# Kernel optimization log

Measured on AMD Instinct MI355X. Metric: run time of the kernel, lower is better.

Reference implementation:

```python
import jax, jax.numpy as jnp
import numpy as np

IN_CHANNELS = 192
KERNEL_SIZE = 3
GROUPS = 1
N_ITER = 3  # power_it_niter


def _gram_conv(K):
    """Gram step of the conv operator: G[a, b] = sum_o corr(K[o, a], K[o, b]).

    K: (co, ci, k, k) -> (ci, ci, 2k-1, 2k-1). This is the kernel of M^T M
    where M is the (zero-padded) conv operator with kernel K.
    """
    k = K.shape[-1]
    lhs = jnp.transpose(K, (1, 0, 2, 3))  # batch = a-index, channels = o
    rhs = jnp.transpose(K, (1, 0, 2, 3))  # out-chan = b-index, in-chan = o
    return jax.lax.conv_general_dilated(
        lhs, rhs, window_strides=(1, 1),
        padding=[(k - 1, k - 1), (k - 1, k - 1)],
        dimension_numbers=("NCHW", "OIHW", "NCHW"))


def _sigma_one_group(K, n_iter):
    """Gram-iteration spectral-norm estimate (Delattre et al. 2024).

    sigma(K_0) ~= prod_t f_t^(1/2^t) * ||K_T||_F^(1/2^T), f_t = Frobenius norm
    before each Gram squaring (normalization keeps values in fp range).
    """
    log_sigma = jnp.asarray(0.0, K.dtype)
    for t in range(n_iter):  # static unroll: kernel spatial size grows k -> 2k-1
        f = jnp.sqrt(jnp.sum(K * K))
        K = K / f
        log_sigma = log_sigma + jnp.log(f) / (2.0 ** t)
        K = _gram_conv(K)
    f_final = jnp.sqrt(jnp.sum(K * K))
    log_sigma = log_sigma + jnp.log(f_final) / (2.0 ** n_iter)
    return jnp.exp(log_sigma)


def compute_delattre2024(K, n_iter):
    # K: (groups, c, c, k, k) -> (groups,) per-group spectral norm estimates
    return jax.vmap(lambda g: _sigma_one_group(g, n_iter))(K)


def setup_inputs() -> dict:
    key = jax.random.key(0)
    kernel = jax.random.normal(
        key, (IN_CHANNELS * GROUPS, IN_CHANNELS, KERNEL_SIZE, KERNEL_SIZE),
        dtype=jnp.float32)
    return {"kernel": kernel}


def reference(kernel):
    g = GROUPS
    c = IN_CHANNELS // GROUPS
    K = kernel.reshape(g, c, c, KERNEL_SIZE, KERNEL_SIZE)
    sigmas = compute_delattre2024(K, N_ITER)  # (groups,)
    K = K / sigmas.reshape(-1, 1, 1, 1, 1)
    return K.reshape(IN_CHANNELS * GROUPS, IN_CHANNELS, KERNEL_SIZE, KERNEL_SIZE)
```

## Files before the change

### kernel.cpp

```cpp
#include <hip/hip_runtime.h>
#include <hip/hip_bf16.h>

typedef __bf16 bf16;
typedef __attribute__((ext_vector_type(8))) __bf16 bf16x8;
typedef __attribute__((ext_vector_type(4))) float f32x4;
typedef __attribute__((ext_vector_type(4))) int i32x4;

#define CH 192
#define MAT (CH * CH)
#define NF 145
#define FSTRIDE (2 * MAT)
#define NELEM (CH * CH * 9)
#define XSCALE 9.765625e-4f
#define W17 0.36959913571644626f
#define NGRAM (8 * 19 * 3)


__global__ void k_dft(const float* __restrict__ K, bf16* __restrict__ X,
                      float* __restrict__ s3) {
    __shared__ float twc[17], tws[17];
    int bid = blockIdx.x;
    int xcd = bid & 7;
    int r = bid >> 3;
    int g = r / 18, chunk = r % 18;
    int t = threadIdx.x;
    if (bid == 0 && t == 0) *s3 = 0.0f;
    if (t < 17) {
        float s, c;
        __sincosf(-W17 * (float)t, &s, &c);
        twc[t] = c; tws[t] = s;
    }
    int p0 = chunk * 2048 + t * 8;
    int a = p0 / CH, o0 = p0 % CH;
    float kv[8][9];
#pragma unroll
    for (int j = 0; j < 8; ++j) {
        const float* src = K + ((size_t)(o0 + j) * CH + a) * 9;
#pragma unroll
        for (int i = 0; i < 9; ++i) kv[j][i] = src[i];
    }
    __syncthreads();
#pragma unroll
    for (int u = 0; u < 5; ++u) {
        int f = xcd + 8 * (g * 5 + u);
        if (f >= NF) continue;
        int fy, fx;
        if (f < 9) { fy = 0; fx = f; }
        else { int uu = f - 9; fy = 1 + uu / 17; fx = uu % 17; }
        float pyr = twc[fy], pyi = tws[fy];
        float pxr = twc[fx], pxi = tws[fx];
        int fx2 = 2 * fx; if (fx2 >= 17) fx2 -= 17;
        int fy2 = 2 * fy; if (fy2 >= 17) fy2 -= 17;
        float px2r = twc[fx2], px2i = tws[fx2];
        float py2r = twc[fy2], py2i = tws[fy2];
        bf16x8 vr, vi;
#pragma unroll
        for (int j = 0; j < 8; ++j) {
            float s0r = kv[j][0] + kv[j][1] * pxr + kv[j][2] * px2r, s0i = kv[j][1] * pxi + kv[j][2] * px2i;
            float s1r = kv[j][3] + kv[j][4] * pxr + kv[j][5] * px2r, s1i = kv[j][4] * pxi + kv[j][5] * px2i;
            float s2r = kv[j][6] + kv[j][7] * pxr + kv[j][8] * px2r, s2i = kv[j][7] * pxi + kv[j][8] * px2i;
            float ar = s0r + pyr * s1r - pyi * s1i + py2r * s2r - py2i * s2i;
            float ai = s0i + pyr * s1i + pyi * s1r + py2r * s2i + py2i * s2r;
            vr[j] = (bf16)(ar * XSCALE);
            vi[j] = (bf16)(ai * XSCALE);
        }
        size_t base = (size_t)f * FSTRIDE + p0;
        *(i32x4*)(X + base)       = __builtin_bit_cast(i32x4, vr);
        *(i32x4*)(X + base + MAT) = __builtin_bit_cast(i32x4, vi);
    }
}

#define LDSR 104
#define SLAB (96 * LDSR)
#define DLDSR 200
#define DSLAB (96 * DLDSR)
#define OLDSR 104

#define COMPUTE_KS(STRIDE, SSIZE, SB2, KO_BASE)                                       \
    {                                                                                 \
        bf16x8 ar[3], ai[3], nai[3], br[3], bi[3];                                    \
        int ko = (KO_BASE) + kq;                                                      \
        _Pragma("unroll")                                                             \
        for (int mt = 0; mt < 3; ++mt) {                                              \
            ar[mt] = *(const bf16x8*)&lds[0 * (SSIZE) + (wr + mt * 16 + ml) * (STRIDE) + ko]; \
            ai[mt] = *(const bf16x8*)&lds[1 * (SSIZE) + (wr + mt * 16 + ml) * (STRIDE) + ko]; \
            br[mt] = *(const bf16x8*)&lds[((SB2) + 0) * (SSIZE) + (wc + mt * 16 + ml) * (STRIDE) + ko]; \
            bi[mt] = *(const bf16x8*)&lds[((SB2) + 1) * (SSIZE) + (wc + mt * 16 + ml) * (STRIDE) + ko]; \
            i32x4 uu = __builtin_bit_cast(i32x4, ai[mt]);                             \
            uu ^= 0x80008000;                                                         \
            nai[mt] = __builtin_bit_cast(bf16x8, uu);                                 \
        }                                                                             \
        _Pragma("unroll")                                                             \
        for (int mt = 0; mt < 3; ++mt)                                                \
            _Pragma("unroll")                                                         \
            for (int nt = 0; nt < 3; ++nt) {                                          \
                cr[mt][nt] = __builtin_amdgcn_mfma_f32_16x16x32_bf16(ar[mt],  br[nt], cr[mt][nt], 0, 0, 0); \
                cr[mt][nt] = __builtin_amdgcn_mfma_f32_16x16x32_bf16(ai[mt],  bi[nt], cr[mt][nt], 0, 0, 0); \
                ci[mt][nt] = __builtin_amdgcn_mfma_f32_16x16x32_bf16(ar[mt],  bi[nt], ci[mt][nt], 0, 0, 0); \
                ci[mt][nt] = __builtin_amdgcn_mfma_f32_16x16x32_bf16(nai[mt], br[nt], ci[mt][nt], 0, 0, 0); \
            }                                                                         \
    }

template <bool WRITE, bool NORM>
__global__ __launch_bounds__(256, 2) void k_gram(const bf16* __restrict__ X,
                                                 bf16* __restrict__ Y,
                                                 float* __restrict__ s3) {
    __shared__ bf16 lds[4 * SLAB];
    __shared__ float red[4];
    int bid = blockIdx.x;
    int xcd = bid & 7, r = bid >> 3;
    int fi = r / 3, q = r % 3;
    int f = xcd + 8 * fi;
    if (f >= NF) return;
    int row0 = (q == 2) ? 96 : 0;
    int col0 = (q >= 1) ? 96 : 0;
    bool diag = (q != 1);
    const bf16* Xf = X + (size_t)f * FSTRIDE;

    int tid = threadIdx.x;
    int lane = tid & 63, w = tid >> 6;
    int wr = (w >> 1) * 48, wc = (w & 1) * 48;
    int ml = lane & 15, kq = (lane >> 4) * 8;

    f32x4 cr[3][3], ci[3][3];
#pragma unroll
    for (int i = 0; i < 3; ++i)
#pragma unroll
        for (int j = 0; j < 3; ++j) {
            cr[i][j] = f32x4{0.f, 0.f, 0.f, 0.f};
            ci[i][j] = f32x4{0.f, 0.f, 0.f, 0.f};
        }

    if (diag) {
        i32x4 v[18];
#pragma unroll
        for (int s = 0; s < 2; ++s) {
            const bf16* src = Xf + (s ? MAT : 0) + (size_t)row0 * CH;
#pragma unroll
            for (int j = 0; j < 9; ++j) {
                int c = j * 256 + tid;
                int rr = c / 24, cc = c % 24;
                v[s * 9 + j] = *(const i32x4*)(src + rr * CH + cc * 8);
            }
        }
#pragma unroll
        for (int s = 0; s < 2; ++s)
#pragma unroll
            for (int j = 0; j < 9; ++j) {
                int c = j * 256 + tid;
                int rr = c / 24, cc = c % 24;
                *(i32x4*)&lds[s * DSLAB + rr * DLDSR + cc * 8] = v[s * 9 + j];
            }
        __syncthreads();
#pragma unroll
        for (int ks = 0; ks < 192; ks += 32) {
            COMPUTE_KS(DLDSR, DSLAB, 0, ks)
        }
    } else {
#pragma unroll
        for (int ph = 0; ph < 2; ++ph) {
            int kc = ph * 96;
            i32x4 v[18];
#pragma unroll
            for (int j = 0; j < 18; ++j) {
                int gi = j * 256 + tid;
                int s = gi / 1152, c = gi % 1152;
                int rr = c / 12, cc = c % 12;
                const bf16* src = Xf + ((s & 1) ? MAT : 0)
                                + (size_t)(((s < 2) ? row0 : col0) + rr) * CH + kc;
                v[j] = *(const i32x4*)(src + cc * 8);
            }
            __syncthreads();
#pragma unroll
            for (int j = 0; j < 18; ++j) {
                int gi = j * 256 + tid;
                int s = gi / 1152, c = gi % 1152;
                int rr = c / 12, cc = c % 12;
                *(i32x4*)&lds[s * SLAB + rr * LDSR + cc * 8] = v[j];
            }
            __syncthreads();
#pragma unroll
            for (int ks = 0; ks < 96; ks += 32) {
                COMPUTE_KS(LDSR, SLAB, 2, ks)
            }
        }
    }

    if (WRITE) {
        bf16* tileA = lds;
        bf16* tileB = lds + 96 * OLDSR;
        bf16* Yf = Y + (size_t)f * FSTRIDE;
        int lr0 = wr + (lane >> 4) * 4;
        int lc0 = wc + ml;
#pragma unroll
        for (int part = 0; part < 2; ++part) {
            __syncthreads();
#pragma unroll
            for (int mt = 0; mt < 3; ++mt)
#pragma unroll
                for (int nt = 0; nt < 3; ++nt)
#pragma unroll
                    for (int rr = 0; rr < 4; ++rr) {
                        float vv = part ? ci[mt][nt][rr] : cr[mt][nt][rr];
                        int rrow = lr0 + mt * 16 + rr;
                        int ccol = lc0 + nt * 16;
                        tileA[rrow * OLDSR + ccol] = (bf16)vv;
                        if (q == 1)
                            tileB[ccol * OLDSR + rrow] = (bf16)(part ? -vv : vv);
                    }
            __syncthreads();
            bf16* dst = Yf + (part ? MAT : 0) + (size_t)row0 * CH + col0;
            for (int ch = tid; ch < 96 * 12; ch += 256) {
                int rw = ch / 12, cc = ch % 12;
                *(i32x4*)&dst[(size_t)rw * CH + cc * 8] = *(const i32x4*)&tileA[rw * OLDSR + cc * 8];
            }
            if (q == 1) {
                bf16* dst2 = Yf + (part ? MAT : 0) + (size_t)col0 * CH + row0;
                for (int ch = tid; ch < 96 * 12; ch += 256) {
                    int rw = ch / 12, cc = ch % 12;
                    *(i32x4*)&dst2[(size_t)rw * CH + cc * 8] = *(const i32x4*)&tileB[rw * OLDSR + cc * 8];
                }
            }
        }
    }
    if (NORM) {
        float loc = 0.f;
#pragma unroll
        for (int mt = 0; mt < 3; ++mt)
#pragma unroll
            for (int nt = 0; nt < 3; ++nt)
#pragma unroll
                for (int rr = 0; rr < 4; ++rr)
                    loc += cr[mt][nt][rr] * cr[mt][nt][rr] + ci[mt][nt][rr] * ci[mt][nt][rr];
#pragma unroll
        for (int off = 32; off > 0; off >>= 1) loc += __shfl_down(loc, off, 64);
        if (lane == 0) red[w] = loc;
        __syncthreads();
        if (tid == 0) {
            float base = (f == 0) ? 1.0f : 2.0f;
            float wq = (q == 1) ? 2.0f : 1.0f;
            atomicAdd(s3, base * wq * (red[0] + red[1] + red[2] + red[3]));
        }
    }
}

__global__ void k_scale(const float* __restrict__ K, float* __restrict__ out,
                        const float* __restrict__ s3) {
    float sig = 1024.0f * exp2f(log2f((*s3) * (1.0f / 289.0f)) * 0.0625f);
    float inv = 1.0f / sig;
    int i = (blockIdx.x * 256 + threadIdx.x) * 4;
    f32x4 v = *(const f32x4*)(K + i);
    v *= inv;
    *(f32x4*)(out + i) = v;
}

extern "C" void kernel_launch(void* const* d_in, const int* in_sizes, int n_in,
                              void* d_out, int out_size, void* d_ws, size_t ws_size,
                              hipStream_t stream) {
    const float* K = (const float*)d_in[0];
    float* out = (float*)d_out;
    char* ws = (char*)d_ws;
    float* s3 = (float*)ws;
    bf16* bufX = (bf16*)(ws + 256);
    bf16* bufH = bufX + (size_t)NF * FSTRIDE;

    k_dft<<<8 * 4 * 18, 256, 0, stream>>>(K, bufX, s3);
    k_gram<true,  false><<<NGRAM, 256, 0, stream>>>(bufX, bufH, nullptr);
    k_gram<true,  false><<<NGRAM, 256, 0, stream>>>(bufH, bufX, nullptr);
    k_gram<false, true ><<<NGRAM, 256, 0, stream>>>(bufX, nullptr, s3);
    k_scale<<<NELEM / 1024, 256, 0, stream>>>(K, out, s3);
}
```

Before: 113.2 us.

## Fuse three Gram-squaring launches into one per-frequency kernel with LDS-resident matrices

```diff
diff --git a/kernel.cpp b/kernel.cpp
--- a/kernel.cpp
+++ b/kernel.cpp
@@ -13,7 +13,6 @@
 #define NELEM (CH * CH * 9)
 #define XSCALE 9.765625e-4f
 #define W17 0.36959913571644626f
-#define NGRAM (8 * 19 * 3)
 
 
 __global__ void k_dft(const float* __restrict__ K, bf16* __restrict__ X,
@@ -70,177 +69,145 @@
     }
 }
 
-#define LDSR 104
-#define SLAB (96 * LDSR)
-#define DLDSR 200
-#define DSLAB (96 * DLDSR)
-#define OLDSR 104
-
-#define COMPUTE_KS(STRIDE, SSIZE, SB2, KO_BASE)                                       \
-    {                                                                                 \
-        bf16x8 ar[3], ai[3], nai[3], br[3], bi[3];                                    \
-        int ko = (KO_BASE) + kq;                                                      \
-        _Pragma("unroll")                                                             \
-        for (int mt = 0; mt < 3; ++mt) {                                              \
-            ar[mt] = *(const bf16x8*)&lds[0 * (SSIZE) + (wr + mt * 16 + ml) * (STRIDE) + ko]; \
-            ai[mt] = *(const bf16x8*)&lds[1 * (SSIZE) + (wr + mt * 16 + ml) * (STRIDE) + ko]; \
-            br[mt] = *(const bf16x8*)&lds[((SB2) + 0) * (SSIZE) + (wc + mt * 16 + ml) * (STRIDE) + ko]; \
-            bi[mt] = *(const bf16x8*)&lds[((SB2) + 1) * (SSIZE) + (wc + mt * 16 + ml) * (STRIDE) + ko]; \
-            i32x4 uu = __builtin_bit_cast(i32x4, ai[mt]);                             \
-            uu ^= 0x80008000;                                                         \
-            nai[mt] = __builtin_bit_cast(bf16x8, uu);                                 \
-        }                                                                             \
-        _Pragma("unroll")                                                             \
-        for (int mt = 0; mt < 3; ++mt)                                                \
-            _Pragma("unroll")                                                         \
-            for (int nt = 0; nt < 3; ++nt) {                                          \
-                cr[mt][nt] = __builtin_amdgcn_mfma_f32_16x16x32_bf16(ar[mt],  br[nt], cr[mt][nt], 0, 0, 0); \
-                cr[mt][nt] = __builtin_amdgcn_mfma_f32_16x16x32_bf16(ai[mt],  bi[nt], cr[mt][nt], 0, 0, 0); \
-                ci[mt][nt] = __builtin_amdgcn_mfma_f32_16x16x32_bf16(ar[mt],  bi[nt], ci[mt][nt], 0, 0, 0); \
-                ci[mt][nt] = __builtin_amdgcn_mfma_f32_16x16x32_bf16(nai[mt], br[nt], ci[mt][nt], 0, 0, 0); \
-            }                                                                         \
-    }
-
-template <bool WRITE, bool NORM>
-__global__ __launch_bounds__(256, 2) void k_gram(const bf16* __restrict__ X,
-                                                 bf16* __restrict__ Y,
-                                                 float* __restrict__ s3) {
-    __shared__ bf16 lds[4 * SLAB];
-    __shared__ float red[4];
-    int bid = blockIdx.x;
-    int xcd = bid & 7, r = bid >> 3;
-    int fi = r / 3, q = r % 3;
-    int f = xcd + 8 * fi;
-    if (f >= NF) return;
-    int row0 = (q == 2) ? 96 : 0;
-    int col0 = (q >= 1) ? 96 : 0;
-    bool diag = (q != 1);
+#define S3S 200
+#define SLAB3 (192 * S3S)
+
+__global__ __launch_bounds__(512, 2) void k_g3(const bf16* __restrict__ X,
+                                               float* __restrict__ s3) {
+    __shared__ __align__(16) bf16 lds[2 * SLAB3];
+    __shared__ float red[8];
+    int f = blockIdx.x;
     const bf16* Xf = X + (size_t)f * FSTRIDE;
-
     int tid = threadIdx.x;
     int lane = tid & 63, w = tid >> 6;
-    int wr = (w >> 1) * 48, wc = (w & 1) * 48;
     int ml = lane & 15, kq = (lane >> 4) * 8;
-
-    f32x4 cr[3][3], ci[3][3];
-#pragma unroll
-    for (int i = 0; i < 3; ++i)
-#pragma unroll
-        for (int j = 0; j < 3; ++j) {
-            cr[i][j] = f32x4{0.f, 0.f, 0.f, 0.f};
-            ci[i][j] = f32x4{0.f, 0.f, 0.f, 0.f};
+    int rb  = (w >> 1) * 48;
+    int cb1 = ((w & 1) | ((w >> 1) & 2)) * 48;
+    int cb2 = cb1 + 96;
+    bool two = (w < 4);
+
+    {
+        i32x4 v[18];
+#pragma unroll
+        for (int s = 0; s < 2; ++s)
+#pragma unroll
+            for (int j = 0; j < 9; ++j) {
+                int c = j * 512 + tid;
+                int rr = c / 24, cc = c % 24;
+                v[s * 9 + j] = *(const i32x4*)(Xf + (s ? MAT : 0) + rr * CH + cc * 8);
+            }
+#pragma unroll
+        for (int s = 0; s < 2; ++s)
+#pragma unroll
+            for (int j = 0; j < 9; ++j) {
+                int c = j * 512 + tid;
+                int rr = c / 24, cc = c % 24;
+                *(i32x4*)&lds[s * SLAB3 + rr * S3S + cc * 8] = v[s * 9 + j];
+            }
+    }
+    __syncthreads();
+
+    f32x4 cr1[3][3], ci1[3][3], cr2[3][3], ci2[3][3];
+#pragma unroll 1
+    for (int round = 0; round < 3; ++round) {
+#pragma unroll
+        for (int i = 0; i < 3; ++i)
+#pragma unroll
+            for (int j = 0; j < 3; ++j) {
+                cr1[i][j] = f32x4{0.f, 0.f, 0.f, 0.f};
+                ci1[i][j] = f32x4{0.f, 0.f, 0.f, 0.f};
+                cr2[i][j] = f32x4{0.f, 0.f, 0.f, 0.f};
+                ci2[i][j] = f32x4{0.f, 0.f, 0.f, 0.f};
+            }
+#pragma unroll
+        for (int ks = 0; ks < 192; ks += 32) {
+            int ko = ks + kq;
+            bf16x8 ar[3], ai[3], nai[3];
+#pragma unroll
+            for (int mt = 0; mt < 3; ++mt) {
+                ar[mt] = *(const bf16x8*)&lds[(rb + mt * 16 + ml) * S3S + ko];
+                ai[mt] = *(const bf16x8*)&lds[SLAB3 + (rb + mt * 16 + ml) * S3S + ko];
+                i32x4 u = __builtin_bit_cast(i32x4, ai[mt]);
+                u ^= 0x80008000;
+                nai[mt] = __builtin_bit_cast(bf16x8, u);
+            }
+#pragma unroll
+            for (int nt = 0; nt < 3; ++nt) {
+                bf16x8 br = *(const bf16x8*)&lds[(cb1 + nt * 16 + ml) * S3S + ko];
+                bf16x8 bi = *(const bf16x8*)&lds[SLAB3 + (cb1 + nt * 16 + ml) * S3S + ko];
+#pragma unroll
+                for (int mt = 0; mt < 3; ++mt) {
+                    cr1[mt][nt] = __builtin_amdgcn_mfma_f32_16x16x32_bf16(ar[mt],  br, cr1[mt][nt], 0, 0, 0);
+                    cr1[mt][nt] = __builtin_amdgcn_mfma_f32_16x16x32_bf16(ai[mt],  bi, cr1[mt][nt], 0, 0, 0);
+                    ci1[mt][nt] = __builtin_amdgcn_mfma_f32_16x16x32_bf16(ar[mt],  bi, ci1[mt][nt], 0, 0, 0);
+                    ci1[mt][nt] = __builtin_amdgcn_mfma_f32_16x16x32_bf16(nai[mt], br, ci1[mt][nt], 0, 0, 0);
+                }
+                if (two) {
+                    bf16x8 br2 = *(const bf16x8*)&lds[(cb2 + nt * 16 + ml) * S3S + ko];
+                    bf16x8 bi2 = *(const bf16x8*)&lds[SLAB3 + (cb2 + nt * 16 + ml) * S3S + ko];
+#pragma unroll
+                    for (int mt = 0; mt < 3; ++mt) {
+                        cr2[mt][nt] = __builtin_amdgcn_mfma_f32_16x16x32_bf16(ar[mt],  br2, cr2[mt][nt], 0, 0, 0);
+                        cr2[mt][nt] = __builtin_amdgcn_mfma_f32_16x16x32_bf16(ai[mt],  bi2, cr2[mt][nt], 0, 0, 0);
+                        ci2[mt][nt] = __builtin_amdgcn_mfma_f32_16x16x32_bf16(ar[mt],  bi2, ci2[mt][nt], 0, 0, 0);
+                        ci2[mt][nt] = __builtin_amdgcn_mfma_f32_16x16x32_bf16(nai[mt], br2, ci2[mt][nt], 0, 0, 0);
+                    }
+                }
+            }
         }
-
-    if (diag) {
-        i32x4 v[18];
-#pragma unroll
-        for (int s = 0; s < 2; ++s) {
-            const bf16* src = Xf + (s ? MAT : 0) + (size_t)row0 * CH;
-#pragma unroll
-            for (int j = 0; j < 9; ++j) {
-                int c = j * 256 + tid;
-                int rr = c / 24, cc = c % 24;
-                v[s * 9 + j] = *(const i32x4*)(src + rr * CH + cc * 8);
-            }
-        }
-#pragma unroll
-        for (int s = 0; s < 2; ++s)
-#pragma unroll
-            for (int j = 0; j < 9; ++j) {
-                int c = j * 256 + tid;
-                int rr = c / 24, cc = c % 24;
-                *(i32x4*)&lds[s * DSLAB + rr * DLDSR + cc * 8] = v[s * 9 + j];
-            }
-        __syncthreads();
-#pragma unroll
-        for (int ks = 0; ks < 192; ks += 32) {
-            COMPUTE_KS(DLDSR, DSLAB, 0, ks)
-        }
-    } else {
-#pragma unroll
-        for (int ph = 0; ph < 2; ++ph) {
-            int kc = ph * 96;
-            i32x4 v[18];
-#pragma unroll
-            for (int j = 0; j < 18; ++j) {
-                int gi = j * 256 + tid;
-                int s = gi / 1152, c = gi % 1152;
-                int rr = c / 12, cc = c % 12;
-                const bf16* src = Xf + ((s & 1) ? MAT : 0)
-                                + (size_t)(((s < 2) ? row0 : col0) + rr) * CH + kc;
-                v[j] = *(const i32x4*)(src + cc * 8);
-            }
+        if (round < 2) {
             __syncthreads();
-#pragma unroll
-            for (int j = 0; j < 18; ++j) {
-                int gi = j * 256 + tid;
-                int s = gi / 1152, c = gi % 1152;
-                int rr = c / 12, cc = c % 12;
-                *(i32x4*)&lds[s * SLAB + rr * LDSR + cc * 8] = v[j];
-            }
-            __syncthreads();
-#pragma unroll
-            for (int ks = 0; ks < 96; ks += 32) {
-                COMPUTE_KS(LDSR, SLAB, 2, ks)
-            }
-        }
-    }
-
-    if (WRITE) {
-        bf16* tileA = lds;
-        bf16* tileB = lds + 96 * OLDSR;
-        bf16* Yf = Y + (size_t)f * FSTRIDE;
-        int lr0 = wr + (lane >> 4) * 4;
-        int lc0 = wc + ml;
-#pragma unroll
-        for (int part = 0; part < 2; ++part) {
-            __syncthreads();
+            int lr = (lane >> 4) * 4;
 #pragma unroll
             for (int mt = 0; mt < 3; ++mt)
 #pragma unroll
                 for (int nt = 0; nt < 3; ++nt)
 #pragma unroll
                     for (int rr = 0; rr < 4; ++rr) {
-                        float vv = part ? ci[mt][nt][rr] : cr[mt][nt][rr];
-                        int rrow = lr0 + mt * 16 + rr;
-                        int ccol = lc0 + nt * 16;
-                        tileA[rrow * OLDSR + ccol] = (bf16)vv;
-                        if (q == 1)
-                            tileB[ccol * OLDSR + rrow] = (bf16)(part ? -vv : vv);
+                        int row = rb + mt * 16 + lr + rr;
+                        int c1 = cb1 + nt * 16 + ml;
+                        lds[row * S3S + c1]         = (bf16)cr1[mt][nt][rr];
+                        lds[SLAB3 + row * S3S + c1] = (bf16)ci1[mt][nt][rr];
+                        if (two) {
+                            int c2 = cb2 + nt * 16 + ml;
+                            float vr = cr2[mt][nt][rr], vi = ci2[mt][nt][rr];
+                            lds[row * S3S + c2]         = (bf16)vr;
+                            lds[SLAB3 + row * S3S + c2] = (bf16)vi;
+                            lds[c2 * S3S + row]         = (bf16)vr;
+                            lds[SLAB3 + c2 * S3S + row] = (bf16)(-vi);
+                        }
                     }
             __syncthreads();
-            bf16* dst = Yf + (part ? MAT : 0) + (size_t)row0 * CH + col0;
-            for (int ch = tid; ch < 96 * 12; ch += 256) {
-                int rw = ch / 12, cc = ch % 12;
-                *(i32x4*)&dst[(size_t)rw * CH + cc * 8] = *(const i32x4*)&tileA[rw * OLDSR + cc * 8];
-            }
-            if (q == 1) {
-                bf16* dst2 = Yf + (part ? MAT : 0) + (size_t)col0 * CH + row0;
-                for (int ch = tid; ch < 96 * 12; ch += 256) {
-                    int rw = ch / 12, cc = ch % 12;
-                    *(i32x4*)&dst2[(size_t)rw * CH + cc * 8] = *(const i32x4*)&tileB[rw * OLDSR + cc * 8];
-                }
-            }
         }
     }
-    if (NORM) {
-        float loc = 0.f;
+
+    float loc = 0.f;
+#pragma unroll
+    for (int mt = 0; mt < 3; ++mt)
+#pragma unroll
+        for (int nt = 0; nt < 3; ++nt)
+#pragma unroll
+            for (int rr = 0; rr < 4; ++rr)
+                loc += cr1[mt][nt][rr] * cr1[mt][nt][rr] + ci1[mt][nt][rr] * ci1[mt][nt][rr];
+    if (two) {
+        float l2 = 0.f;
 #pragma unroll
         for (int mt = 0; mt < 3; ++mt)
 #pragma unroll
             for (int nt = 0; nt < 3; ++nt)
 #pragma unroll
                 for (int rr = 0; rr < 4; ++rr)
-                    loc += cr[mt][nt][rr] * cr[mt][nt][rr] + ci[mt][nt][rr] * ci[mt][nt][rr];
-#pragma unroll
-        for (int off = 32; off > 0; off >>= 1) loc += __shfl_down(loc, off, 64);
-        if (lane == 0) red[w] = loc;
-        __syncthreads();
-        if (tid == 0) {
-            float base = (f == 0) ? 1.0f : 2.0f;
-            float wq = (q == 1) ? 2.0f : 1.0f;
-            atomicAdd(s3, base * wq * (red[0] + red[1] + red[2] + red[3]));
-        }
+                    l2 += cr2[mt][nt][rr] * cr2[mt][nt][rr] + ci2[mt][nt][rr] * ci2[mt][nt][rr];
+        loc += 2.0f * l2;
+    }
+#pragma unroll
+    for (int off = 32; off > 0; off >>= 1) loc += __shfl_down(loc, off, 64);
+    if (lane == 0) red[w] = loc;
+    __syncthreads();
+    if (tid == 0) {
+        float base = (f == 0) ? 1.0f : 2.0f;
+        atomicAdd(s3, base * (red[0] + red[1] + red[2] + red[3] +
+                              red[4] + red[5] + red[6] + red[7]));
     }
 }
 
@@ -262,11 +229,8 @@
     char* ws = (char*)d_ws;
     float* s3 = (float*)ws;
     bf16* bufX = (bf16*)(ws + 256);
-    bf16* bufH = bufX + (size_t)NF * FSTRIDE;
 
     k_dft<<<8 * 4 * 18, 256, 0, stream>>>(K, bufX, s3);
-    k_gram<true,  false><<<NGRAM, 256, 0, stream>>>(bufX, bufH, nullptr);
-    k_gram<true,  false><<<NGRAM, 256, 0, stream>>>(bufH, bufX, nullptr);
-    k_gram<false, true ><<<NGRAM, 256, 0, stream>>>(bufX, nullptr, s3);
+    k_g3<<<NF, 512, 0, stream>>>(bufX, s3);
     k_scale<<<NELEM / 1024, 256, 0, stream>>>(K, out, s3);
 }
```

New measurement: 178.4 us. 1.58x slower.
